# Kernel optimization log

Hardware: AMD Instinct MI355X
Metric: run time of the kernel (lower is better)

## Reference

```python
import jax, jax.numpy as jnp
import numpy as np

B_, L_, DM = 8, 1024, 256
DS, DC, EX = 16, 4, 2
DI = EX * DM            # d_inner = 512
DTR = max(1, DM // 16)  # dt_rank = 16


def setup_inputs() -> dict:
    key = jax.random.key(0)
    ks = iter(jax.random.split(key, 40))
    def n(shape, s=0.02):
        return jax.random.normal(next(ks), shape, jnp.float32) * s
    inp = {"x": jax.random.normal(next(ks), (B_, L_, DM), jnp.float32)}
    inp["norm_g"] = jnp.ones((DM,), jnp.float32)
    inp["norm_b"] = jnp.zeros((DM,), jnp.float32)
    for m in ("f", "b"):
        inp[f"inW_{m}"] = n((DM, 2 * DI))
        inp[f"convW_{m}"] = n((DI, DC))
        inp[f"convB_{m}"] = jnp.zeros((DI,), jnp.float32)
        inp[f"xW_{m}"] = n((DI, DTR + 2 * DS))
        inp[f"dtW_{m}"] = n((DTR, DI))
        inp[f"dtB_{m}"] = jnp.zeros((DI,), jnp.float32)
        # ALog init: log of [1..dState] repeated over dInner rows
        inp[f"ALog_{m}"] = jnp.log(jnp.tile(jnp.arange(1, DS + 1, dtype=jnp.float32), (DI, 1)))
        inp[f"Dp_{m}"] = jnp.ones((DI,), jnp.float32)
        inp[f"outW_{m}"] = n((DI, DM))
    inp["fusW"] = n((2 * DM, DM))
    inp["fusB"] = jnp.zeros((DM,), jnp.float32)
    return inp


def _dw_conv(x, w, b):
    # causal depthwise conv1d: x [B,L,DI], w [DI,DC] -> [B,L,DI]
    xc = jnp.transpose(x, (0, 2, 1))  # B,DI,L
    out = jax.lax.conv_general_dilated(
        xc, w[:, None, :], window_strides=(1,), padding=[(DC - 1, 0)],
        dimension_numbers=("NCH", "OIH", "NCH"), feature_group_count=DI)
    return jnp.transpose(out + b[:, None], (0, 2, 1))


def _ssm(x, xW, dtW, dtB, ALog, Dp):
    # x: [B,L,DI]
    A = -jnp.exp(ALog)                                   # [DI,DS]
    xdbl = x @ xW                                        # [B,L,DTR+2*DS]
    dlt, Bp, Cp = jnp.split(xdbl, [DTR, DTR + DS], axis=-1)
    delta = jax.nn.softplus(dlt @ dtW + dtB)             # [B,L,DI]
    dA = jnp.exp(delta[..., None] * A)                   # [B,L,DI,DS]
    dBx = (delta * x)[..., None] * Bp[:, :, None, :]     # [B,L,DI,DS]

    def step(h, t):
        a, bb, c = t
        h = a * h + bb                                   # [B,DI,DS]
        y = jnp.einsum('bdn,bn->bd', h, c)
        return h, y

    h0 = jnp.zeros((x.shape[0], DI, DS), x.dtype)
    _, ys = jax.lax.scan(step, h0, (jnp.moveaxis(dA, 1, 0),
                                    jnp.moveaxis(dBx, 1, 0),
                                    jnp.moveaxis(Cp, 1, 0)))
    return jnp.moveaxis(ys, 0, 1) + Dp * x               # [B,L,DI]


def _mamba(x, inW, convW, convB, xW, dtW, dtB, ALog, Dp, outW):
    xr = x @ inW                                         # [B,L,2*DI]
    xs, res = jnp.split(xr, 2, axis=-1)
    xs = jax.nn.silu(_dw_conv(xs, convW, convB))
    y = _ssm(xs, xW, dtW, dtB, ALog, Dp)
    return (y * jax.nn.silu(res)) @ outW                 # [B,L,DM]


def reference(x, norm_g, norm_b,
              inW_f, convW_f, convB_f, xW_f, dtW_f, dtB_f, ALog_f, Dp_f, outW_f,
              inW_b, convW_b, convB_b, xW_b, dtW_b, dtB_b, ALog_b, Dp_b, outW_b,
              fusW, fusB):
    # LayerNorm
    mu = x.mean(-1, keepdims=True)
    var = ((x - mu) ** 2).mean(-1, keepdims=True)
    xn = (x - mu) * jax.lax.rsqrt(var + 1e-5) * norm_g + norm_b
    # forward-direction Mamba
    xf = _mamba(xn, inW_f, convW_f, convB_f, xW_f, dtW_f, dtB_f, ALog_f, Dp_f, outW_f)
    # backward-direction Mamba (flip along time)
    xb = _mamba(jnp.flip(xn, 1), inW_b, convW_b, convB_b, xW_b, dtW_b, dtB_b, ALog_b, Dp_b, outW_b)
    xb = jnp.flip(xb, 1)
    fused = jnp.concatenate([xf, xb], axis=-1) @ fusW + fusB
    return x + fused  # dropout is identity in eval
```

## Files before the change

### kernel.cpp

```cpp
#include <hip/hip_runtime.h>
#include <cmath>

typedef __bf16 bf16x8 __attribute__((ext_vector_type(8)));
typedef float  f32x4  __attribute__((ext_vector_type(4)));
typedef float  f32x2  __attribute__((ext_vector_type(2)));

#define B_  8
#define L_  1024
#define DM  256
#define DI  512
#define DS  16
#define DTR 16
#define M_  (B_*L_)
#define NC  64
#define CT  16

__device__ inline float softplus_f(float z){
  return (z > 20.f) ? z : __logf(1.f + __expf(z));
}
__device__ inline float silu_f(float z){
  return z / (1.f + __expf(-z));
}

__device__ inline void pow_tree(float e1, float* p){
  float e2=e1*e1, e4=e2*e2, e8=e4*e4;
  float e3=e2*e1, e5=e4*e1, e6=e4*e2, e7=e4*e3;
  p[0]=e1;  p[1]=e2;  p[2]=e3;  p[3]=e4;
  p[4]=e5;  p[5]=e6;  p[6]=e7;  p[7]=e8;
  p[8]=e8*e1;  p[9]=e8*e2;  p[10]=e8*e3;  p[11]=e8*e4;
  p[12]=e8*e5; p[13]=e8*e6; p[14]=e8*e7;  p[15]=e8*e8;
}

__global__ __launch_bounds__(256) void probe_k(const void* x, int* flag){
  __shared__ int sbad[256];
  int tid = threadIdx.x;
  const unsigned short* u = (const unsigned short*)x;
  int bad = 0;
  for (int i = tid; i < 4096; i += 256){
    unsigned short v = u[2*i];
    int e = (v >> 7) & 0xFF;
    if (e >= 160 || e < 96) bad++;
  }
  sbad[tid] = bad;
  __syncthreads();
  if (tid == 0){
    int t = 0;
    for (int i=0;i<256;i++) t += sbad[i];
    *flag = (t > 1024) ? 1 : 0;
  }
}

struct PrepJob { const void* src; void* dst; int rows; int cols; int f32out; };
struct PrepArgs { PrepJob j[26]; int nj; };

__global__ __launch_bounds__(256) void prep_k(PrepArgs a, const int* flag){
  int e = blockIdx.x*256 + threadIdx.x;
  const int f = *flag;
  #pragma unroll 1
  for (int jj=0; jj<a.nj; jj++){
    int sz = a.j[jj].rows * a.j[jj].cols;
    if (e < sz){
      int cols = a.j[jj].cols;
      int r = e / cols, c = e - r*cols;
      float v = f ? ((const float*)a.j[jj].src)[e] : (float)((const __bf16*)a.j[jj].src)[e];
      if (a.j[jj].f32out) ((float*)a.j[jj].dst)[c*a.j[jj].rows + r] = v;
      else ((__bf16*)a.j[jj].dst)[(long)c*a.j[jj].rows + r] = (__bf16)v;
      return;
    }
    e -= sz;
  }
}

__global__ __launch_bounds__(256) void ln_k(const void* x, const __bf16* g,
                                            const __bf16* bb, __bf16* xn, const int* flag){
  const int row = blockIdx.x;
  const int d = threadIdx.x;
  const int f = *flag;
  long idx = (long)row*DM + d;
  float v = f ? ((const float*)x)[idx] : (float)(((const __bf16*)x)[idx]);
  float s = v, q = v*v;
  #pragma unroll
  for (int off=32; off>0; off>>=1){
    s += __shfl_down(s, off);
    q += __shfl_down(q, off);
  }
  __shared__ float ss[4], sq[4];
  int w = d >> 6, ln = d & 63;
  if (ln == 0){ ss[w] = s; sq[w] = q; }
  __syncthreads();
  s = ss[0]+ss[1]+ss[2]+ss[3];
  q = sq[0]+sq[1]+sq[2]+sq[3];
  float mu  = s * (1.f/DM);
  float var = q * (1.f/DM) - mu*mu;
  float xnv = (v - mu) * rsqrtf(var + 1e-5f) * (float)g[d] + (float)bb[d];
  xn[idx] = (__bf16)xnv;
}

template<int BM,int BN,int KK>
__global__ __launch_bounds__(256) void gemm_in_k(
    const __bf16* A, const __bf16* B0, const __bf16* B1,
    __bf16* xz0, __bf16* xz1, __bf16* res0, __bf16* res1,
    int lda, int ldb)
{
  constexpr int TM = BM/2, TN = BN/2;
  constexpr int WMT = TM/16, WNT = TN/16;
  constexpr int LA = BM/64, LB = BN/64;

  const int dir = blockIdx.z;
  const __bf16* Bt = dir ? B1 : B0;
  __bf16* xz  = dir ? xz1 : xz0;
  __bf16* res = dir ? res1 : res0;
  const int tid  = threadIdx.x;
  const int lane = tid & 63;
  const int wid  = tid >> 6;
  const int wm = wid & 1;
  const int wn = wid >> 1;
  const int mBase = blockIdx.x * BM;
  const int nBase = blockIdx.y * BN;
  const int lm = lane & 15;
  const int kq = (lane >> 4) * 8;

  __shared__ __bf16 As[BM*32];
  __shared__ __bf16 Bs[BN*32];

  const __bf16* aS[LA];
  const __bf16* bS[LB];
  {
    int colk = (tid & 3) * 8;
    #pragma unroll
    for (int ld=0; ld<LA; ld++){
      int r = mBase + ld*64 + (tid >> 2);
      if (dir==1){ int b = r >> 10, t = r & (L_-1); r = (b<<10) + (L_-1-t); }
      aS[ld] = A + (long)r*lda + colk;
    }
    #pragma unroll
    for (int ld=0; ld<LB; ld++){
      int r = nBase + ld*64 + (tid >> 2);
      bS[ld] = Bt + (long)r*ldb + colk;
    }
  }

  f32x4 acc[WMT][WNT] = {};
  for (int k0=0; k0<KK; k0+=32){
    #pragma unroll
    for (int ld=0; ld<LA; ld++)
      __builtin_amdgcn_global_load_lds(
        (const __attribute__((address_space(1))) void*)(aS[ld] + k0),
        (__attribute__((address_space(3))) void*)(&As[ld*2048 + tid*8]), 16, 0, 0);
    #pragma unroll
    for (int ld=0; ld<LB; ld++)
      __builtin_amdgcn_global_load_lds(
        (const __attribute__((address_space(1))) void*)(bS[ld] + k0),
        (__attribute__((address_space(3))) void*)(&Bs[ld*2048 + tid*8]), 16, 0, 0);
    __syncthreads();
    bf16x8 af[WMT], bfr[WNT];
    #pragma unroll
    for (int i=0;i<WMT;i++) af[i]  = *(const bf16x8*)&As[(wm*TM + i*16 + lm)*32 + kq];
    #pragma unroll
    for (int j=0;j<WNT;j++) bfr[j] = *(const bf16x8*)&Bs[(wn*TN + j*16 + lm)*32 + kq];
    #pragma unroll
    for (int i=0;i<WMT;i++)
      #pragma unroll
      for (int j=0;j<WNT;j++)
        acc[i][j] = __builtin_amdgcn_mfma_f32_16x16x32_bf16(af[i], bfr[j], acc[i][j], 0,0,0);
    __syncthreads();
  }

  #pragma unroll
  for (int i=0;i<WMT;i++){
    #pragma unroll
    for (int rr=0;rr<4;rr++){
      int r = mBase + wm*TM + i*16 + (lane>>4)*4 + rr;
      #pragma unroll
      for (int j=0;j<WNT;j++){
        int c = nBase + wn*TN + j*16 + lm;
        float v = acc[i][j][rr];
        if (c < DI) xz[(long)r*DI + c] = (__bf16)v;
        else        res[(long)r*DI + (c-DI)] = (__bf16)v;
      }
    }
  }
}

template<int BM,int BN,int KK>
__global__ __launch_bounds__(256) void gemm_fin_k(
    const __bf16* Af, const __bf16* Ab,
    const __bf16* Bt0, const __bf16* Bt1,
    void* Cout, const __bf16* bias, const void* resid, const int* outflag)
{
  constexpr int TM = BM/2, TN = BN/2;
  constexpr int WMT = TM/16, WNT = TN/16;
  constexpr int LA = BM/64, LB = BN/64;

  const int tid  = threadIdx.x;
  const int lane = tid & 63;
  const int wid  = tid >> 6;
  const int wm = wid & 1;
  const int wn = wid >> 1;
  const int mBase = blockIdx.x * BM;
  const int nBase = blockIdx.y * BN;
  const int lm = lane & 15;
  const int kq = (lane >> 4) * 8;
  const int of = outflag ? *outflag : 0;

  __shared__ __bf16 As[BM*32];
  __shared__ __bf16 Bs[BN*32];

  f32x4 acc[WMT][WNT] = {};
  #pragma unroll 1
  for (int dd=0; dd<2; dd++){
    const __bf16* A  = dd ? Ab  : Af;
    const __bf16* Bt = dd ? Bt1 : Bt0;
    const __bf16* aS[LA];
    const __bf16* bS[LB];
    {
      int colk = (tid & 3) * 8;
      #pragma unroll
      for (int ld=0; ld<LA; ld++){
        int r = mBase + ld*64 + (tid >> 2);
        if (dd==1){ int b = r >> 10, t = r & (L_-1); r = (b<<10) + (L_-1-t); }
        aS[ld] = A + (long)r*DI + colk;
      }
      #pragma unroll
      for (int ld=0; ld<LB; ld++){
        int r = nBase + ld*64 + (tid >> 2);
        bS[ld] = Bt + (long)r*DI + colk;
      }
    }
    for (int k0=0; k0<KK; k0+=32){
      #pragma unroll
      for (int ld=0; ld<LA; ld++)
        __builtin_amdgcn_global_load_lds(
          (const __attribute__((address_space(1))) void*)(aS[ld] + k0),
          (__attribute__((address_space(3))) void*)(&As[ld*2048 + tid*8]), 16, 0, 0);
      #pragma unroll
      for (int ld=0; ld<LB; ld++)
        __builtin_amdgcn_global_load_lds(
          (const __attribute__((address_space(1))) void*)(bS[ld] + k0),
          (__attribute__((address_space(3))) void*)(&Bs[ld*2048 + tid*8]), 16, 0, 0);
      __syncthreads();
      bf16x8 af[WMT], bfr[WNT];
      #pragma unroll
      for (int i=0;i<WMT;i++) af[i]  = *(const bf16x8*)&As[(wm*TM + i*16 + lm)*32 + kq];
      #pragma unroll
      for (int j=0;j<WNT;j++) bfr[j] = *(const bf16x8*)&Bs[(wn*TN + j*16 + lm)*32 + kq];
      #pragma unroll
      for (int i=0;i<WMT;i++)
        #pragma unroll
        for (int j=0;j<WNT;j++)
          acc[i][j] = __builtin_amdgcn_mfma_f32_16x16x32_bf16(af[i], bfr[j], acc[i][j], 0,0,0);
      __syncthreads();
    }
  }

  #pragma unroll
  for (int i=0;i<WMT;i++){
    #pragma unroll
    for (int rr=0;rr<4;rr++){
      int r = mBase + wm*TM + i*16 + (lane>>4)*4 + rr;
      #pragma unroll
      for (int j=0;j<WNT;j++){
        int c = nBase + wn*TN + j*16 + lm;
        float v = acc[i][j][rr];
        float rsd = of ? ((const float*)resid)[(long)r*DM + c]
                       : (float)((const __bf16*)resid)[(long)r*DM + c];
        v += (float)bias[c] + rsd;
        if (of) ((float*)Cout)[(long)r*DM + c] = v;
        else    ((__bf16*)Cout)[(long)r*DM + c] = (__bf16)v;
      }
    }
  }
}

template<int WMT,int WNT,int BWM,int BWN,int KK,int BF16OUT>
__global__ __launch_bounds__(64*BWM*BWN) void gemm_r_k(
    const __bf16* A0, const __bf16* A1,
    const __bf16* B0, const __bf16* B1,
    void* C0, void* C1,
    int lda, int ldb, int ldc)
{
  const int dir = blockIdx.z;
  const __bf16* A  = dir ? A1 : A0;
  const __bf16* Bt = dir ? B1 : B0;
  void* C = dir ? C1 : C0;
  const int tid  = threadIdx.x;
  const int lane = tid & 63;
  const int wid  = tid >> 6;
  const int wm = wid % BWM;
  const int wn = wid / BWM;
  const int mBase = (blockIdx.x*BWM + wm) * (WMT*16);
  const int nBase = (blockIdx.y*BWN + wn) * (WNT*16);
  const int lm = lane & 15;
  const int kq = (lane >> 4) * 8;

  long aoff[WMT];
  #pragma unroll
  for (int i=0;i<WMT;i++) aoff[i] = (long)(mBase + i*16 + lm) * lda + kq;
  long boff[WNT];
  #pragma unroll
  for (int j=0;j<WNT;j++) boff[j] = (long)(nBase + j*16 + lm) * ldb + kq;

  f32x4 acc[WMT][WNT] = {};
  #pragma unroll
  for (int k0=0; k0<KK; k0+=32){
    bf16x8 af[WMT], bfr[WNT];
    #pragma unroll
    for (int i=0;i<WMT;i++) af[i]  = *(const bf16x8*)(A  + aoff[i] + k0);
    #pragma unroll
    for (int j=0;j<WNT;j++) bfr[j] = *(const bf16x8*)(Bt + boff[j] + k0);
    #pragma unroll
    for (int i=0;i<WMT;i++)
      #pragma unroll
      for (int j=0;j<WNT;j++)
        acc[i][j] = __builtin_amdgcn_mfma_f32_16x16x32_bf16(af[i], bfr[j], acc[i][j], 0,0,0);
  }

  #pragma unroll
  for (int i=0;i<WMT;i++)
    #pragma unroll
    for (int rr=0;rr<4;rr++){
      int r = mBase + i*16 + (lane>>4)*4 + rr;
      #pragma unroll
      for (int j=0;j<WNT;j++){
        int c = nBase + j*16 + lm;
        if (BF16OUT) ((__bf16*)C)[(long)r*ldc + c] = (__bf16)acc[i][j][rr];
        else         ((float*)C)[(long)r*ldc + c] = acc[i][j][rr];
      }
    }
}

__global__ __launch_bounds__(256) void conv_k(
    const __bf16* xz0, const __bf16* xz1,
    const float* cw0, const float* cw1,
    const __bf16* cb0, const __bf16* cb1,
    __bf16* xs0, __bf16* xs1)
{
  const int dir = blockIdx.z;
  const __bf16* xz = dir ? xz1 : xz0;
  const float*  cw = dir ? cw1 : cw0;
  const __bf16* cb = dir ? cb1 : cb0;
  __bf16* xs = dir ? xs1 : xs0;

  int gid = blockIdx.x*256 + threadIdx.x;
  int c8 = gid & 63;
  int t  = (gid >> 6) & (L_-1);
  int b  = gid >> 16;
  int cbase = c8*8;

  float acc[8];
  bf16x8 bb = *(const bf16x8*)(cb + cbase);
  #pragma unroll
  for (int c=0;c<8;c++) acc[c] = (float)bb[c];
  #pragma unroll
  for (int j=0;j<4;j++){
    int tj = t - 3 + j;
    if (tj >= 0){
      bf16x8 xv = *(const bf16x8*)(xz + ((long)(b*L_ + tj))*DI + cbase);
      #pragma unroll
      for (int c=0;c<8;c++) acc[c] += (float)xv[c] * cw[j*DI + cbase + c];
    }
  }
  bf16x8 outv;
  #pragma unroll
  for (int c=0;c<8;c++) outv[c] = (__bf16)silu_f(acc[c]);
  *(bf16x8*)(xs + ((long)(b*L_ + t))*DI + cbase) = outv;
}

__global__ __launch_bounds__(256) void dt_k(
    const float* xd0, const float* xd1,
    const float* dw0, const float* dw1,
    const __bf16* dtB0, const __bf16* dtB1,
    float* dg0, float* dg1)
{
  const int dir = blockIdx.z;
  const float*  xd  = dir ? xd1 : xd0;
  const float*  dw  = dir ? dw1 : dw0;
  const __bf16* dtB = dir ? dtB1 : dtB0;
  float* dg = dir ? dg1 : dg0;
  const long row0 = (long)blockIdx.x * 32;
  const int tid = threadIdx.x;

  __shared__ float sdlt[32][16];
  { int e = tid*2; int r = e>>4, q = e&15;
    *(f32x2*)&sdlt[r][q] = *(const f32x2*)(xd + (row0+r)*48 + q); }

  const int d0 = tid, d1 = tid + 256;
  float dwa[16], dwb[16];
  { const f32x4* p = (const f32x4*)(dw + d0*DTR);
    #pragma unroll
    for (int q=0;q<4;q++){ f32x4 v=p[q]; dwa[q*4]=v[0]; dwa[q*4+1]=v[1]; dwa[q*4+2]=v[2]; dwa[q*4+3]=v[3]; } }
  { const f32x4* p = (const f32x4*)(dw + d1*DTR);
    #pragma unroll
    for (int q=0;q<4;q++){ f32x4 v=p[q]; dwb[q*4]=v[0]; dwb[q*4+1]=v[1]; dwb[q*4+2]=v[2]; dwb[q*4+3]=v[3]; } }
  const float b0v = (float)dtB[d0];
  const float b1v = (float)dtB[d1];
  __syncthreads();

  #pragma unroll 4
  for (int r=0;r<32;r++){
    f32x4 q0 = *(const f32x4*)&sdlt[r][0];
    f32x4 q1 = *(const f32x4*)&sdlt[r][4];
    f32x4 q2 = *(const f32x4*)&sdlt[r][8];
    f32x4 q3 = *(const f32x4*)&sdlt[r][12];
    float z0 = b0v, z1 = b1v;
    z0 += q0[0]*dwa[0]+q0[1]*dwa[1]+q0[2]*dwa[2]+q0[3]*dwa[3];
    z0 += q1[0]*dwa[4]+q1[1]*dwa[5]+q1[2]*dwa[6]+q1[3]*dwa[7];
    z0 += q2[0]*dwa[8]+q2[1]*dwa[9]+q2[2]*dwa[10]+q2[3]*dwa[11];
    z0 += q3[0]*dwa[12]+q3[1]*dwa[13]+q3[2]*dwa[14]+q3[3]*dwa[15];
    z1 += q0[0]*dwb[0]+q0[1]*dwb[1]+q0[2]*dwb[2]+q0[3]*dwb[3];
    z1 += q1[0]*dwb[4]+q1[1]*dwb[5]+q1[2]*dwb[6]+q1[3]*dwb[7];
    z1 += q2[0]*dwb[8]+q2[1]*dwb[9]+q2[2]*dwb[10]+q2[3]*dwb[11];
    z1 += q3[0]*dwb[12]+q3[1]*dwb[13]+q3[2]*dwb[14]+q3[3]*dwb[15];
    dg[(row0+r)*DI + d0] = softplus_f(z0);
    dg[(row0+r)*DI + d1] = softplus_f(z1);
  }
}

__global__ __launch_bounds__(256) void scanA_k(
    const float* xd0, const float* xd1,
    const __bf16* xs0, const __bf16* xs1,
    const float* dg0, const float* dg1,
    const float* ALf0, const float* ALf1,
    float* hend, float* sumd)
{
  const int dir = blockIdx.z;
  const float*  xd  = dir ? xd1 : xd0;
  const __bf16* xs  = dir ? xs1 : xs0;
  const float*  dg  = dir ? dg1 : dg0;
  const float*  ALf = dir ? ALf1 : ALf0;

  const int b   = blockIdx.y;
  const int c   = blockIdx.x >> 1;
  const int dg_ = blockIdx.x & 1;
  const int tid = threadIdx.x;
  const int d   = dg_*256 + tid;
  const int db  = dir*8 + b;
  const long row0 = (long)b*L_ + c*CT;

  __shared__ float sB[CT][16];
  if (tid < CT*4){ int e = tid*4; int t = e>>4, n = e&15;
    *(f32x4*)&sB[t][n] = *(const f32x4*)(xd + (row0+t)*48 + 16 + n); }

  float A[16];
  { const f32x4* p = (const f32x4*)(ALf + d*DS);
    #pragma unroll
    for (int q=0;q<4;q++){ f32x4 v=p[q];
      A[q*4]=-__expf(v[0]); A[q*4+1]=-__expf(v[1]); A[q*4+2]=-__expf(v[2]); A[q*4+3]=-__expf(v[3]); } }
  bool pow_ok = true;
  #pragma unroll
  for (int n=0;n<16;n++) pow_ok = pow_ok && (fabsf(A[n] + (float)(n+1)) < 0.003f*(n+1));

  float h[16];
  #pragma unroll
  for (int n=0;n<16;n++) h[n]=0.f;
  float sdelta = 0.f;
  __syncthreads();

  if (pow_ok){
    #pragma unroll 2
    for (int t=0;t<CT;t++){
      long row = row0 + t;
      f32x4 b0 = *(const f32x4*)&sB[t][0];
      f32x4 b1 = *(const f32x4*)&sB[t][4];
      f32x4 b2 = *(const f32x4*)&sB[t][8];
      f32x4 b3 = *(const f32x4*)&sB[t][12];
      float delta = dg[row*DI + d];
      sdelta += delta;
      float xv = (float)xs[row*DI + d];
      float dx = delta*xv;
      float pw[16];
      pow_tree(__expf(-delta), pw);
      float Bv[16] = {b0[0],b0[1],b0[2],b0[3], b1[0],b1[1],b1[2],b1[3],
                      b2[0],b2[1],b2[2],b2[3], b3[0],b3[1],b3[2],b3[3]};
      #pragma unroll
      for (int n=0;n<16;n++)
        h[n] = pw[n]*h[n] + dx*Bv[n];
    }
  } else {
    #pragma unroll 2
    for (int t=0;t<CT;t++){
      long row = row0 + t;
      f32x4 b0 = *(const f32x4*)&sB[t][0];
      f32x4 b1 = *(const f32x4*)&sB[t][4];
      f32x4 b2 = *(const f32x4*)&sB[t][8];
      f32x4 b3 = *(const f32x4*)&sB[t][12];
      float delta = dg[row*DI + d];
      sdelta += delta;
      float xv = (float)xs[row*DI + d];
      float dx = delta*xv;
      float Bv[16] = {b0[0],b0[1],b0[2],b0[3], b1[0],b1[1],b1[2],b1[3],
                      b2[0],b2[1],b2[2],b2[3], b3[0],b3[1],b3[2],b3[3]};
      #pragma unroll
      for (int n=0;n<16;n++)
        h[n] = __expf(delta*A[n])*h[n] + dx*Bv[n];
    }
  }

  long hb = (((long)db*NC + c)*DI + d)*16;
  f32x4* hp = (f32x4*)(hend + hb);
  #pragma unroll
  for (int q=0;q<4;q++){ f32x4 v; v[0]=h[q*4]; v[1]=h[q*4+1]; v[2]=h[q*4+2]; v[3]=h[q*4+3]; hp[q]=v; }
  sumd[((long)db*NC + c)*DI + d] = sdelta;
}

__global__ __launch_bounds__(256) void scanB_k(
    const float* ALf0, const float* ALf1,
    const float* hend, const float* sumd, float* Hbuf)
{
  int gid = blockIdx.x*256 + threadIdx.x;
  int n  = gid & 15;
  int d  = (gid>>4) & 511;
  int db = gid >> 13;
  const float* ALf = (db>=8) ? ALf1 : ALf0;
  float A_dn = -__expf(ALf[d*DS + n]);
  float H = 0.f;
  #pragma unroll 1
  for (int c=0;c<NC;c++){
    long base = (((long)db*NC + c)*DI + d)*16 + n;
    Hbuf[base] = H;
    float S = sumd[((long)db*NC + c)*DI + d];
    H = hend[base] + __expf(A_dn*S)*H;
  }
}

__global__ __launch_bounds__(256) void scanC_k(
    const float* xd0, const float* xd1,
    const __bf16* xs0, const __bf16* xs1,
    __bf16* res0, __bf16* res1,
    const float* dg0, const float* dg1,
    const float* ALf0, const float* ALf1,
    const __bf16* Dp0, const __bf16* Dp1,
    const float* Hbuf)
{
  const int dir = blockIdx.z;
  const float*  xd  = dir ? xd1 : xd0;
  const __bf16* xs  = dir ? xs1 : xs0;
  __bf16*       res = dir ? res1 : res0;
  const float*  dg  = dir ? dg1 : dg0;
  const float*  ALf = dir ? ALf1 : ALf0;
  const __bf16* Dp  = dir ? Dp1 : Dp0;

  const int b   = blockIdx.y;
  const int c   = blockIdx.x >> 1;
  const int dg_ = blockIdx.x & 1;
  const int tid = threadIdx.x;
  const int d   = dg_*256 + tid;
  const int db  = dir*8 + b;
  const long row0 = (long)b*L_ + c*CT;

  __shared__ float sBC[CT][32];
  if (tid < CT*8){ int e = tid*4; int t = e>>5, cc = e&31;
    *(f32x4*)&sBC[t][cc] = *(const f32x4*)(xd + (row0+t)*48 + 16 + cc); }

  float A[16];
  { const f32x4* p = (const f32x4*)(ALf + d*DS);
    #pragma unroll
    for (int q=0;q<4;q++){ f32x4 v=p[q];
      A[q*4]=-__expf(v[0]); A[q*4+1]=-__expf(v[1]); A[q*4+2]=-__expf(v[2]); A[q*4+3]=-__expf(v[3]); } }
  bool pow_ok = true;
  #pragma unroll
  for (int n=0;n<16;n++) pow_ok = pow_ok && (fabsf(A[n] + (float)(n+1)) < 0.003f*(n+1));

  float h[16];
  { long hb = (((long)db*NC + c)*DI + d)*16;
    const f32x4* p = (const f32x4*)(Hbuf + hb);
    #pragma unroll
    for (int q=0;q<4;q++){ f32x4 v = p[q]; h[q*4]=v[0]; h[q*4+1]=v[1]; h[q*4+2]=v[2]; h[q*4+3]=v[3]; } }
  const float Dpv = (float)Dp[d];
  __syncthreads();

  if (pow_ok){
    #pragma unroll 2
    for (int t=0;t<CT;t++){
      long row = row0 + t;
      f32x4 b0 = *(const f32x4*)&sBC[t][0];
      f32x4 b1 = *(const f32x4*)&sBC[t][4];
      f32x4 b2 = *(const f32x4*)&sBC[t][8];
      f32x4 b3 = *(const f32x4*)&sBC[t][12];
      f32x4 c0 = *(const f32x4*)&sBC[t][16];
      f32x4 c1 = *(const f32x4*)&sBC[t][20];
      f32x4 c2 = *(const f32x4*)&sBC[t][24];
      f32x4 c3 = *(const f32x4*)&sBC[t][28];
      float delta = dg[row*DI + d];
      float xv = (float)xs[row*DI + d];
      float dx = delta*xv;
      float pw[16];
      pow_tree(__expf(-delta), pw);
      float Bv[16] = {b0[0],b0[1],b0[2],b0[3], b1[0],b1[1],b1[2],b1[3],
                      b2[0],b2[1],b2[2],b2[3], b3[0],b3[1],b3[2],b3[3]};
      float Cv[16] = {c0[0],c0[1],c0[2],c0[3], c1[0],c1[1],c1[2],c1[3],
                      c2[0],c2[1],c2[2],c2[3], c3[0],c3[1],c3[2],c3[3]};
      float p = 0.f;
      #pragma unroll
      for (int n=0;n<16;n++){
        h[n] = pw[n]*h[n] + dx*Bv[n];
        p += h[n]*Cv[n];
      }
      float yv = p + Dpv*xv;
      float rv = (float)res[row*DI + d];
      res[row*DI + d] = (__bf16)(yv * silu_f(rv));
    }
  } else {
    #pragma unroll 2
    for (int t=0;t<CT;t++){
      long row = row0 + t;
      f32x4 b0 = *(const f32x4*)&sBC[t][0];
      f32x4 b1 = *(const f32x4*)&sBC[t][4];
      f32x4 b2 = *(const f32x4*)&sBC[t][8];
      f32x4 b3 = *(const f32x4*)&sBC[t][12];
      f32x4 c0 = *(const f32x4*)&sBC[t][16];
      f32x4 c1 = *(const f32x4*)&sBC[t][20];
      f32x4 c2 = *(const f32x4*)&sBC[t][24];
      f32x4 c3 = *(const f32x4*)&sBC[t][28];
      float delta = dg[row*DI + d];
      float xv = (float)xs[row*DI + d];
      float dx = delta*xv;
      float Bv[16] = {b0[0],b0[1],b0[2],b0[3], b1[0],b1[1],b1[2],b1[3],
                      b2[0],b2[1],b2[2],b2[3], b3[0],b3[1],b3[2],b3[3]};
      float Cv[16] = {c0[0],c0[1],c0[2],c0[3], c1[0],c1[1],c1[2],c1[3],
                      c2[0],c2[1],c2[2],c2[3], c3[0],c3[1],c3[2],c3[3]};
      float p = 0.f;
      #pragma unroll
      for (int n=0;n<16;n++){
        h[n] = __expf(delta*A[n])*h[n] + dx*Bv[n];
        p += h[n]*Cv[n];
      }
      float yv = p + Dpv*xv;
      float rv = (float)res[row*DI + d];
      res[row*DI + d] = (__bf16)(yv * silu_f(rv));
    }
  }
}

__global__ __launch_bounds__(256) void scan_k(
    const float* xd0, const float* xd1,
    const __bf16* xs0, const __bf16* xs1,
    __bf16* res0, __bf16* res1,
    const float* dw0, const float* dw1,
    const __bf16* dtB0, const __bf16* dtB1,
    const __bf16* AL0, const __bf16* AL1,
    const __bf16* Dp0, const __bf16* Dp1)
{
  const int dir = blockIdx.z;
  const float*  xd  = dir ? xd1 : xd0;
  const __bf16* xs  = dir ? xs1 : xs0;
  __bf16*       res = dir ? res1 : res0;
  const float*  dw  = dir ? dw1 : dw0;
  const __bf16* dtB = dir ? dtB1 : dtB0;
  const __bf16* AL  = dir ? AL1 : AL0;
  const __bf16* Dp  = dir ? Dp1 : Dp0;

  const int b  = blockIdx.y;
  const int dt = blockIdx.x;
  const int tid = threadIdx.x;
  const int n  = tid & 15;
  const int dl = tid >> 4;
  const int d  = dt*16 + dl;

  __shared__ float sxd[128][48];
  __shared__ float sx[128][16];
  __shared__ float sdelta[128][16];
  __shared__ float sy[128][16];
  __shared__ float sdw[16][17];
  __shared__ float sdb[16];

  sdw[dl][n] = dw[(dt*16+dl)*DTR + n];
  if (tid < 16) sdb[tid] = (float)dtB[dt*16 + tid];
  const float A_dn = -__expf((float)AL[d*DS + n]);
  float h = 0.f;
  __syncthreads();

  const long rowB = (long)b * L_;
  for (int c0=0; c0<L_; c0+=128){
    #pragma unroll 1
    for (int k=0;k<24;k++){
      int e = tid + k*256;
      int t = e / 48, col = e - t*48;
      sxd[t][col] = xd[(rowB + c0 + t)*48 + col];
    }
    #pragma unroll 1
    for (int k=0;k<8;k++){
      int e = tid + k*256;
      int t = e >> 4, dc = e & 15;
      sx[t][dc] = (float)xs[(rowB + c0 + t)*DI + dt*16 + dc];
    }
    __syncthreads();
    #pragma unroll 1
    for (int k=0;k<8;k++){
      int e = tid + k*256;
      int t = e >> 4, dc = e & 15;
      float z = sdb[dc];
      #pragma unroll
      for (int q=0;q<16;q++) z += sxd[t][q] * sdw[dc][q];
      sdelta[t][dc] = softplus_f(z);
    }
    __syncthreads();
    #pragma unroll 2
    for (int tt=0;tt<128;tt++){
      float delta = sdelta[tt][dl];
      float xv = sx[tt][dl];
      float Bv = sxd[tt][16+n];
      float Cv = sxd[tt][32+n];
      float dA = __expf(delta * A_dn);
      h = dA*h + (delta*xv)*Bv;
      float p = h * Cv;
      p += __shfl_xor(p, 1);
      p += __shfl_xor(p, 2);
      p += __shfl_xor(p, 4);
      p += __shfl_xor(p, 8);
      if (n == 0) sy[tt][dl] = p;
    }
    __syncthreads();
    #pragma unroll 1
    for (int k=0;k<8;k++){
      int e = tid + k*256;
      int t = e >> 4, dc = e & 15;
      long row = rowB + c0 + t;
      float yv = sy[t][dc] + (float)Dp[dt*16+dc] * sx[t][dc];
      float rv = (float)res[row*DI + dt*16 + dc];
      res[row*DI + dt*16 + dc] = (__bf16)(yv * silu_f(rv));
    }
    __syncthreads();
  }
}

extern "C" void kernel_launch(void* const* d_in, const int* in_sizes, int n_in,
                              void* d_out, int out_size, void* d_ws, size_t ws_size,
                              hipStream_t stream)
{
  const size_t MB = 1u<<20;
  if (ws_size < 61*MB) return;
  const bool newscan = (ws_size >= 160*MB);

  char* w = (char*)d_ws;
  __bf16* xz[2]  = {(__bf16*)(w + 0),      (__bf16*)(w + 8*MB)};
  __bf16* res[2] = {(__bf16*)(w + 16*MB),  (__bf16*)(w + 24*MB)};
  __bf16* xsc[2] = {(__bf16*)(w + 32*MB),  (__bf16*)(w + 40*MB)};
  __bf16* xn     = (__bf16*)(w + 48*MB);
  float*  xdbl[2]= {(float*)(w + 48*MB),   (float*)(w + 48*MB + (size_t)M_*48*4)};

  char* wp = w + 52*MB;
  auto carve = [&](size_t bytes)->void*{
    void* p = wp;
    wp += (bytes + 255) & ~(size_t)255;
    return p;
  };
  __bf16 *inWt[2], *xWt[2], *outWr[2], *BtC[2];
  float *dtWt[2], *convWt[2];
  for (int m=0;m<2;m++){
    inWt[m]   = (__bf16*)carve((size_t)(2*DI)*DM*2);
    xWt[m]    = (__bf16*)carve((size_t)48*DI*2);
    outWr[m]  = (__bf16*)carve((size_t)DI*DM*2);
    BtC[m]    = (__bf16*)carve((size_t)DM*DI*2);
    dtWt[m]   = (float*)carve((size_t)DI*DTR*4);
    convWt[m] = (float*)carve((size_t)4*DI*4);
  }
  __bf16* fusWt = (__bf16*)carve((size_t)DM*(2*DM)*2);
  int* flag = (int*)carve(256);
  float* ALf[2] = {(float*)carve((size_t)DI*DS*4), (float*)carve((size_t)DI*DS*4)};

  char* cp = w + 57*MB;
  auto carve2 = [&](size_t elems)->__bf16*{
    __bf16* p = (__bf16*)cp;
    cp += (elems*2 + 255) & ~(size_t)255;
    return p;
  };
  __bf16* ngc = carve2(DM);
  __bf16* nbc = carve2(DM);
  __bf16 *convBc[2], *dtBc[2], *ALc[2], *Dpc[2];
  for (int m=0;m<2;m++){
    convBc[m] = carve2(DI);
    dtBc[m]   = carve2(DI);
    ALc[m]    = carve2((size_t)DI*DS);
    Dpc[m]    = carve2(DI);
  }
  __bf16* fusBc = carve2(DM);

  float* dgA[2] = {(float*)(w + 58*MB), (float*)(w + 74*MB)};
  float* hend = (float*)(w + 90*MB);
  float* sumd = (float*)(w + 124*MB);
  float* Hbuf = (float*)(w + 127*MB);

  probe_k<<<1, 256, 0, stream>>>(d_in[0], flag);

  PrepArgs pa;
  int ji = 0;
  size_t tot = 0;
  auto addj = [&](const void* s, void* dst, int rows, int cols, int f32o){
    pa.j[ji++] = {s, dst, rows, cols, f32o};
    tot += (size_t)rows*cols;
  };
  for (int m=0;m<2;m++){
    int base = 3 + m*9;
    addj(d_in[base+0], inWt[m],  DM,  2*DI, 0);
    addj(d_in[base+3], xWt[m],   DI,  48,   0);
    addj(d_in[base+8], outWr[m], 1,   DI*DM,0);
    addj(d_in[base+4], dtWt[m],  DTR, DI,   1);
    addj(d_in[base+1], convWt[m],DI,  4,    1);
    addj(d_in[base+2], convBc[m],1, DI, 0);
    addj(d_in[base+5], dtBc[m],  1, DI, 0);
    addj(d_in[base+6], ALc[m],   1, DI*DS, 0);
    addj(d_in[base+6], (void*)ALf[m], 1, DI*DS, 1);
    addj(d_in[base+7], Dpc[m],   1, DI, 0);
  }
  addj(d_in[21], fusWt, 2*DM, DM, 0);
  addj(d_in[1],  ngc, 1, DM, 0);
  addj(d_in[2],  nbc, 1, DM, 0);
  addj(d_in[22], fusBc, 1, DM, 0);
  pa.nj = ji;
  prep_k<<<(int)((tot+255)/256), 256, 0, stream>>>(pa, flag);

  gemm_r_k<1,4,4,1,DM,1><<<dim3(4, 8, 2), 256, 0, stream>>>(
      fusWt, fusWt + DM,
      outWr[0], outWr[1], BtC[0], BtC[1], 2*DM, DM, DI);

  ln_k<<<M_, 256, 0, stream>>>(d_in[0], ngc, nbc, xn, flag);
  gemm_in_k<128,128,256><<<dim3(M_/128, (2*DI)/128, 2), 256, 0, stream>>>(
      xn, inWt[0], inWt[1], xz[0], xz[1], res[0], res[1], DM, DM);
  conv_k<<<dim3((M_*64)/256, 1, 2), 256, 0, stream>>>(
      xz[0], xz[1], convWt[0], convWt[1], convBc[0], convBc[1], xsc[0], xsc[1]);
  gemm_r_k<1,3,4,1,DI,0><<<dim3(M_/64, 1, 2), 256, 0, stream>>>(
      xsc[0], xsc[1], xWt[0], xWt[1], xdbl[0], xdbl[1], DI, DI, 48);

  if (newscan){
    dt_k<<<dim3(M_/32, 1, 2), 256, 0, stream>>>(
        xdbl[0], xdbl[1], dtWt[0], dtWt[1], dtBc[0], dtBc[1], dgA[0], dgA[1]);
    scanA_k<<<dim3(NC*2, B_, 2), 256, 0, stream>>>(
        xdbl[0], xdbl[1], xsc[0], xsc[1], dgA[0], dgA[1], ALf[0], ALf[1], hend, sumd);
    scanB_k<<<131072/256, 256, 0, stream>>>(ALf[0], ALf[1], hend, sumd, Hbuf);
    scanC_k<<<dim3(NC*2, B_, 2), 256, 0, stream>>>(
        xdbl[0], xdbl[1], xsc[0], xsc[1], res[0], res[1],
        dgA[0], dgA[1], ALf[0], ALf[1], Dpc[0], Dpc[1], Hbuf);
  } else {
    scan_k<<<dim3(DI/16, B_, 2), 256, 0, stream>>>(
        xdbl[0], xdbl[1], xsc[0], xsc[1], res[0], res[1], dtWt[0], dtWt[1],
        dtBc[0], dtBc[1], ALc[0], ALc[1], Dpc[0], Dpc[1]);
  }

  gemm_fin_k<64,64,DI><<<dim3(M_/64, DM/64, 1), 256, 0, stream>>>(
      res[0], res[1], BtC[0], BtC[1], d_out, fusBc, d_in[0], flag);
}
```

Measured before the change: 283.4 us.

## Inline dtype probe per kernel, split-K x-projection with atomics, drop legacy scan

Removes the separate probe kernel: each kernel now decides fp32 vs bf16 input with a one-wave ballot over the first 64 elements of x. The x-projection GEMM becomes a split-K kernel (four K-chunks) that accumulates into a zeroed fp32 buffer with atomicAdd, which gives more blocks for the skinny 48-column output. The fallback scan path and the unused bf16 ALog copy are dropped, and the launch now requires the larger workspace. The trade-offs are an extra memset, atomic contention on the output, nondeterministic summation order, and a coarser dtype heuristic.

```diff
diff --git a/kernel.cpp b/kernel.cpp
--- a/kernel.cpp
+++ b/kernel.cpp
@@ -31,31 +31,21 @@
   p[12]=e8*e5; p[13]=e8*e6; p[14]=e8*e7;  p[15]=e8*e8;
 }
 
-__global__ __launch_bounds__(256) void probe_k(const void* x, int* flag){
-  __shared__ int sbad[256];
-  int tid = threadIdx.x;
+__device__ inline int flag_from_x(const void* x){
   const unsigned short* u = (const unsigned short*)x;
-  int bad = 0;
-  for (int i = tid; i < 4096; i += 256){
-    unsigned short v = u[2*i];
-    int e = (v >> 7) & 0xFF;
-    if (e >= 160 || e < 96) bad++;
-  }
-  sbad[tid] = bad;
-  __syncthreads();
-  if (tid == 0){
-    int t = 0;
-    for (int i=0;i<256;i++) t += sbad[i];
-    *flag = (t > 1024) ? 1 : 0;
-  }
+  int lane = threadIdx.x & 63;
+  unsigned short v = u[2*lane];
+  int e = (v >> 7) & 0xFF;
+  unsigned long long m = __ballot(e >= 160 || e < 96);
+  return __popcll(m) > 16;
 }
 
 struct PrepJob { const void* src; void* dst; int rows; int cols; int f32out; };
 struct PrepArgs { PrepJob j[26]; int nj; };
 
-__global__ __launch_bounds__(256) void prep_k(PrepArgs a, const int* flag){
+__global__ __launch_bounds__(256) void prep_k(PrepArgs a, const void* xsrc){
+  const int f = flag_from_x(xsrc);
   int e = blockIdx.x*256 + threadIdx.x;
-  const int f = *flag;
   #pragma unroll 1
   for (int jj=0; jj<a.nj; jj++){
     int sz = a.j[jj].rows * a.j[jj].cols;
@@ -72,10 +62,10 @@
 }
 
 __global__ __launch_bounds__(256) void ln_k(const void* x, const __bf16* g,
-                                            const __bf16* bb, __bf16* xn, const int* flag){
+                                            const __bf16* bb, __bf16* xn){
+  const int f = flag_from_x(x);
   const int row = blockIdx.x;
   const int d = threadIdx.x;
-  const int f = *flag;
   long idx = (long)row*DM + d;
   float v = f ? ((const float*)x)[idx] : (float)(((const __bf16*)x)[idx]);
   float s = v, q = v*v;
@@ -186,12 +176,13 @@
 __global__ __launch_bounds__(256) void gemm_fin_k(
     const __bf16* Af, const __bf16* Ab,
     const __bf16* Bt0, const __bf16* Bt1,
-    void* Cout, const __bf16* bias, const void* resid, const int* outflag)
+    void* Cout, const __bf16* bias, const void* resid)
 {
   constexpr int TM = BM/2, TN = BN/2;
   constexpr int WMT = TM/16, WNT = TN/16;
   constexpr int LA = BM/64, LB = BN/64;
 
+  const int of = flag_from_x(resid);
   const int tid  = threadIdx.x;
   const int lane = tid & 63;
   const int wid  = tid >> 6;
@@ -201,7 +192,6 @@
   const int nBase = blockIdx.y * BN;
   const int lm = lane & 15;
   const int kq = (lane >> 4) * 8;
-  const int of = outflag ? *outflag : 0;
 
   __shared__ __bf16 As[BM*32];
   __shared__ __bf16 Bs[BN*32];
@@ -272,17 +262,17 @@
   }
 }
 
-template<int WMT,int WNT,int BWM,int BWN,int KK,int BF16OUT>
+template<int WMT,int WNT,int BWM,int BWN,int KK>
 __global__ __launch_bounds__(64*BWM*BWN) void gemm_r_k(
     const __bf16* A0, const __bf16* A1,
     const __bf16* B0, const __bf16* B1,
-    void* C0, void* C1,
+    __bf16* C0, __bf16* C1,
     int lda, int ldb, int ldc)
 {
   const int dir = blockIdx.z;
   const __bf16* A  = dir ? A1 : A0;
   const __bf16* Bt = dir ? B1 : B0;
-  void* C = dir ? C1 : C0;
+  __bf16* C = dir ? C1 : C0;
   const int tid  = threadIdx.x;
   const int lane = tid & 63;
   const int wid  = tid >> 6;
@@ -323,10 +313,54 @@
       #pragma unroll
       for (int j=0;j<WNT;j++){
         int c = nBase + j*16 + lm;
-        if (BF16OUT) ((__bf16*)C)[(long)r*ldc + c] = (__bf16)acc[i][j][rr];
-        else         ((float*)C)[(long)r*ldc + c] = acc[i][j][rr];
+        C[(long)r*ldc + c] = (__bf16)acc[i][j][rr];
       }
     }
+}
+
+__global__ __launch_bounds__(256) void xproj_k(
+    const __bf16* xs0, const __bf16* xs1,
+    const __bf16* B0, const __bf16* B1,
+    float* xd0, float* xd1)
+{
+  const int dir = blockIdx.z;
+  const __bf16* A  = dir ? xs1 : xs0;
+  const __bf16* Bt = dir ? B1 : B0;
+  float* C = dir ? xd1 : xd0;
+  const int tid  = threadIdx.x;
+  const int lane = tid & 63;
+  const int wid  = tid >> 6;
+  const int mBase = blockIdx.x*64 + wid*16;
+  const int kc = blockIdx.y * 128;
+  const int lm = lane & 15;
+  const int kq = (lane >> 4) * 8;
+
+  long aoff = (long)(mBase + lm)*DI + kc + kq;
+  long boff[3];
+  #pragma unroll
+  for (int j=0;j<3;j++) boff[j] = (long)(j*16 + lm)*DI + kc + kq;
+
+  f32x4 acc[3] = {};
+  #pragma unroll
+  for (int k0=0; k0<128; k0+=32){
+    bf16x8 af = *(const bf16x8*)(A + aoff + k0);
+    bf16x8 bfr[3];
+    #pragma unroll
+    for (int j=0;j<3;j++) bfr[j] = *(const bf16x8*)(Bt + boff[j] + k0);
+    #pragma unroll
+    for (int j=0;j<3;j++)
+      acc[j] = __builtin_amdgcn_mfma_f32_16x16x32_bf16(af, bfr[j], acc[j], 0,0,0);
+  }
+
+  #pragma unroll
+  for (int rr=0;rr<4;rr++){
+    int r = mBase + (lane>>4)*4 + rr;
+    #pragma unroll
+    for (int j=0;j<3;j++){
+      int c = j*16 + lm;
+      atomicAdd(&C[(long)r*48 + c], acc[j][rr]);
+    }
+  }
 }
 
 __global__ __launch_bounds__(256) void conv_k(
@@ -632,105 +666,12 @@
   }
 }
 
-__global__ __launch_bounds__(256) void scan_k(
-    const float* xd0, const float* xd1,
-    const __bf16* xs0, const __bf16* xs1,
-    __bf16* res0, __bf16* res1,
-    const float* dw0, const float* dw1,
-    const __bf16* dtB0, const __bf16* dtB1,
-    const __bf16* AL0, const __bf16* AL1,
-    const __bf16* Dp0, const __bf16* Dp1)
-{
-  const int dir = blockIdx.z;
-  const float*  xd  = dir ? xd1 : xd0;
-  const __bf16* xs  = dir ? xs1 : xs0;
-  __bf16*       res = dir ? res1 : res0;
-  const float*  dw  = dir ? dw1 : dw0;
-  const __bf16* dtB = dir ? dtB1 : dtB0;
-  const __bf16* AL  = dir ? AL1 : AL0;
-  const __bf16* Dp  = dir ? Dp1 : Dp0;
-
-  const int b  = blockIdx.y;
-  const int dt = blockIdx.x;
-  const int tid = threadIdx.x;
-  const int n  = tid & 15;
-  const int dl = tid >> 4;
-  const int d  = dt*16 + dl;
-
-  __shared__ float sxd[128][48];
-  __shared__ float sx[128][16];
-  __shared__ float sdelta[128][16];
-  __shared__ float sy[128][16];
-  __shared__ float sdw[16][17];
-  __shared__ float sdb[16];
-
-  sdw[dl][n] = dw[(dt*16+dl)*DTR + n];
-  if (tid < 16) sdb[tid] = (float)dtB[dt*16 + tid];
-  const float A_dn = -__expf((float)AL[d*DS + n]);
-  float h = 0.f;
-  __syncthreads();
-
-  const long rowB = (long)b * L_;
-  for (int c0=0; c0<L_; c0+=128){
-    #pragma unroll 1
-    for (int k=0;k<24;k++){
-      int e = tid + k*256;
-      int t = e / 48, col = e - t*48;
-      sxd[t][col] = xd[(rowB + c0 + t)*48 + col];
-    }
-    #pragma unroll 1
-    for (int k=0;k<8;k++){
-      int e = tid + k*256;
-      int t = e >> 4, dc = e & 15;
-      sx[t][dc] = (float)xs[(rowB + c0 + t)*DI + dt*16 + dc];
-    }
-    __syncthreads();
-    #pragma unroll 1
-    for (int k=0;k<8;k++){
-      int e = tid + k*256;
-      int t = e >> 4, dc = e & 15;
-      float z = sdb[dc];
-      #pragma unroll
-      for (int q=0;q<16;q++) z += sxd[t][q] * sdw[dc][q];
-      sdelta[t][dc] = softplus_f(z);
-    }
-    __syncthreads();
-    #pragma unroll 2
-    for (int tt=0;tt<128;tt++){
-      float delta = sdelta[tt][dl];
-      float xv = sx[tt][dl];
-      float Bv = sxd[tt][16+n];
-      float Cv = sxd[tt][32+n];
-      float dA = __expf(delta * A_dn);
-      h = dA*h + (delta*xv)*Bv;
-      float p = h * Cv;
-      p += __shfl_xor(p, 1);
-      p += __shfl_xor(p, 2);
-      p += __shfl_xor(p, 4);
-      p += __shfl_xor(p, 8);
-      if (n == 0) sy[tt][dl] = p;
-    }
-    __syncthreads();
-    #pragma unroll 1
-    for (int k=0;k<8;k++){
-      int e = tid + k*256;
-      int t = e >> 4, dc = e & 15;
-      long row = rowB + c0 + t;
-      float yv = sy[t][dc] + (float)Dp[dt*16+dc] * sx[t][dc];
-      float rv = (float)res[row*DI + dt*16 + dc];
-      res[row*DI + dt*16 + dc] = (__bf16)(yv * silu_f(rv));
-    }
-    __syncthreads();
-  }
-}
-
 extern "C" void kernel_launch(void* const* d_in, const int* in_sizes, int n_in,
                               void* d_out, int out_size, void* d_ws, size_t ws_size,
                               hipStream_t stream)
 {
   const size_t MB = 1u<<20;
-  if (ws_size < 61*MB) return;
-  const bool newscan = (ws_size >= 160*MB);
+  if (ws_size < 160*MB) return;
 
   char* w = (char*)d_ws;
   __bf16* xz[2]  = {(__bf16*)(w + 0),      (__bf16*)(w + 8*MB)};
@@ -756,7 +697,6 @@
     convWt[m] = (float*)carve((size_t)4*DI*4);
   }
   __bf16* fusWt = (__bf16*)carve((size_t)DM*(2*DM)*2);
-  int* flag = (int*)carve(256);
   float* ALf[2] = {(float*)carve((size_t)DI*DS*4), (float*)carve((size_t)DI*DS*4)};
 
   char* cp = w + 57*MB;
@@ -767,11 +707,10 @@
   };
   __bf16* ngc = carve2(DM);
   __bf16* nbc = carve2(DM);
-  __bf16 *convBc[2], *dtBc[2], *ALc[2], *Dpc[2];
+  __bf16 *convBc[2], *dtBc[2], *Dpc[2];
   for (int m=0;m<2;m++){
     convBc[m] = carve2(DI);
     dtBc[m]   = carve2(DI);
-    ALc[m]    = carve2((size_t)DI*DS);
     Dpc[m]    = carve2(DI);
   }
   __bf16* fusBc = carve2(DM);
@@ -780,8 +719,6 @@
   float* hend = (float*)(w + 90*MB);
   float* sumd = (float*)(w + 124*MB);
   float* Hbuf = (float*)(w + 127*MB);
-
-  probe_k<<<1, 256, 0, stream>>>(d_in[0], flag);
 
   PrepArgs pa;
   int ji = 0;
@@ -799,7 +736,6 @@
     addj(d_in[base+1], convWt[m],DI,  4,    1);
     addj(d_in[base+2], convBc[m],1, DI, 0);
     addj(d_in[base+5], dtBc[m],  1, DI, 0);
-    addj(d_in[base+6], ALc[m],   1, DI*DS, 0);
     addj(d_in[base+6], (void*)ALf[m], 1, DI*DS, 1);
     addj(d_in[base+7], Dpc[m],   1, DI, 0);
   }
@@ -808,35 +744,30 @@
   addj(d_in[2],  nbc, 1, DM, 0);
   addj(d_in[22], fusBc, 1, DM, 0);
   pa.nj = ji;
-  prep_k<<<(int)((tot+255)/256), 256, 0, stream>>>(pa, flag);
-
-  gemm_r_k<1,4,4,1,DM,1><<<dim3(4, 8, 2), 256, 0, stream>>>(
-      fusWt, fusWt + DM,
-      outWr[0], outWr[1], BtC[0], BtC[1], 2*DM, DM, DI);
-
-  ln_k<<<M_, 256, 0, stream>>>(d_in[0], ngc, nbc, xn, flag);
+  prep_k<<<(int)((tot+255)/256), 256, 0, stream>>>(pa, d_in[0]);
+
+  gemm_r_k<1,4,4,1,DM><<<dim3(4, 8, 2), 256, 0, stream>>>(
+      fusWt, fusWt + DM, outWr[0], outWr[1], BtC[0], BtC[1], 2*DM, DM, DI);
+
+  ln_k<<<M_, 256, 0, stream>>>(d_in[0], ngc, nbc, xn);
   gemm_in_k<128,128,256><<<dim3(M_/128, (2*DI)/128, 2), 256, 0, stream>>>(
       xn, inWt[0], inWt[1], xz[0], xz[1], res[0], res[1], DM, DM);
   conv_k<<<dim3((M_*64)/256, 1, 2), 256, 0, stream>>>(
       xz[0], xz[1], convWt[0], convWt[1], convBc[0], convBc[1], xsc[0], xsc[1]);
-  gemm_r_k<1,3,4,1,DI,0><<<dim3(M_/64, 1, 2), 256, 0, stream>>>(
-      xsc[0], xsc[1], xWt[0], xWt[1], xdbl[0], xdbl[1], DI, DI, 48);
-
-  if (newscan){
-    dt_k<<<dim3(M_/32, 1, 2), 256, 0, stream>>>(
-        xdbl[0], xdbl[1], dtWt[0], dtWt[1], dtBc[0], dtBc[1], dgA[0], dgA[1]);
-    scanA_k<<<dim3(NC*2, B_, 2), 256, 0, stream>>>(
-        xdbl[0], xdbl[1], xsc[0], xsc[1], dgA[0], dgA[1], ALf[0], ALf[1], hend, sumd);
-    scanB_k<<<131072/256, 256, 0, stream>>>(ALf[0], ALf[1], hend, sumd, Hbuf);
-    scanC_k<<<dim3(NC*2, B_, 2), 256, 0, stream>>>(
-        xdbl[0], xdbl[1], xsc[0], xsc[1], res[0], res[1],
-        dgA[0], dgA[1], ALf[0], ALf[1], Dpc[0], Dpc[1], Hbuf);
-  } else {
-    scan_k<<<dim3(DI/16, B_, 2), 256, 0, stream>>>(
-        xdbl[0], xdbl[1], xsc[0], xsc[1], res[0], res[1], dtWt[0], dtWt[1],
-        dtBc[0], dtBc[1], ALc[0], ALc[1], Dpc[0], Dpc[1]);
-  }
+
+  hipMemsetAsync(w + 48*MB, 0, (size_t)M_*48*4*2, stream);
+  xproj_k<<<dim3(M_/64, 4, 2), 256, 0, stream>>>(
+      xsc[0], xsc[1], xWt[0], xWt[1], xdbl[0], xdbl[1]);
+
+  dt_k<<<dim3(M_/32, 1, 2), 256, 0, stream>>>(
+      xdbl[0], xdbl[1], dtWt[0], dtWt[1], dtBc[0], dtBc[1], dgA[0], dgA[1]);
+  scanA_k<<<dim3(NC*2, B_, 2), 256, 0, stream>>>(
+      xdbl[0], xdbl[1], xsc[0], xsc[1], dgA[0], dgA[1], ALf[0], ALf[1], hend, sumd);
+  scanB_k<<<131072/256, 256, 0, stream>>>(ALf[0], ALf[1], hend, sumd, Hbuf);
+  scanC_k<<<dim3(NC*2, B_, 2), 256, 0, stream>>>(
+      xdbl[0], xdbl[1], xsc[0], xsc[1], res[0], res[1],
+      dgA[0], dgA[1], ALf[0], ALf[1], Dpc[0], Dpc[1], Hbuf);
 
   gemm_fin_k<64,64,DI><<<dim3(M_/64, DM/64, 1), 256, 0, stream>>>(
-      res[0], res[1], BtC[0], BtC[1], d_out, fusBc, d_in[0], flag);
-}
+      res[0], res[1], BtC[0], BtC[1], d_out, fusBc, d_in[0]);
+}
```

Result: no change. 285.6 us (+0.8%).
